# Optimization experiments

Measured on AMD Instinct MI355X. Metric: run time of the kernel, lower is better.

Reference implementation:

```python
import jax, jax.numpy as jnp
import numpy as np

B, L, DIN, D = 16, 1024, 512, 1024  # batch, l_max, input_dim, d_model
ORDER = 2


def setup_inputs() -> dict:
    key = jax.random.key(0)
    ks = jax.random.split(key, 8)
    n = lambda i, shape, sc: jax.random.normal(ks[i], shape, dtype=jnp.float32) * sc
    return {
        "x": n(0, (B, L, DIN), 1.0),
        # project_in (Linear since input_dim != output_dim)
        "Wp": n(1, (DIN, D), DIN ** -0.5),
        "bp": jnp.zeros((D,), jnp.float32),
        # hyena in_proj -> (order+1)*d channels
        "W_in": n(2, (D, 3 * D), D ** -0.5),
        "b_in": jnp.zeros((3 * D,), jnp.float32),
        # depthwise causal short conv, kernel 3
        "short_w": n(3, (3 * D, 1, 3), 0.5),
        "short_b": jnp.zeros((3 * D,), jnp.float32),
        # implicit long filters (materialized) + per-channel skip bias
        "k_filt": n(4, (ORDER, L, D), 0.02),
        "D_bias": n(5, (ORDER, D), 1.0),
        # hyena out_proj
        "W_out": n(6, (D, D), D ** -0.5),
        "b_out": jnp.zeros((D,), jnp.float32),
    }


def _fftconv(v, k, d_bias):
    # v: [B, L, d], k: [L, d] -> causal long conv via zero-padded FFT + skip
    n = 2 * v.shape[1]
    vf = jnp.fft.rfft(v.astype(jnp.float32), n=n, axis=1)
    kf = jnp.fft.rfft(k.astype(jnp.float32), n=n, axis=0)
    y = jnp.fft.irfft(vf * kf[None], n=n, axis=1)[:, : v.shape[1]]
    return (y + v * d_bias).astype(v.dtype)


def reference(x, Wp, bp, W_in, b_in, short_w, short_b, k_filt, D_bias, W_out, b_out):
    u = x @ Wp + bp                      # [B, L, D] project_in
    u = u @ W_in + b_in                  # [B, L, 3D]
    # depthwise causal short conv over sequence
    uc = jnp.transpose(u, (0, 2, 1))     # [B, 3D, L]
    uc = jax.lax.conv_general_dilated(
        uc, short_w, window_strides=(1,), padding=[(2, 0)],
        feature_group_count=3 * D, dimension_numbers=("NCH", "OIH", "NCH"),
    )[..., :L] + short_b[None, :, None]
    uc = jnp.transpose(uc, (0, 2, 1))    # [B, L, 3D]
    x1, x2, v = jnp.split(uc, 3, axis=-1)
    # Hyena recurrence: gate then long FFT conv, order=2
    v = _fftconv(v * x2, k_filt[0], D_bias[0])
    v = _fftconv(v * x1, k_filt[1], D_bias[1])
    return v @ W_out + b_out             # [B, L, D]
```

## Files before the change

### kernel.cpp

```cpp
#include <hip/hip_runtime.h>

#define BATCH 16
#define LSEQ 1024
#define DIN 512
#define DMODEL 1024
#define D3 3072
#define KCP 1064

typedef __attribute__((ext_vector_type(4))) float f32x4;
typedef __attribute__((ext_vector_type(8))) short bf16x8;

static __device__ __forceinline__ ushort f2bf(float f) {
    uint u = __float_as_uint(f);
    return (ushort)((u + 0x7FFFu + ((u >> 16) & 1u)) >> 16);
}
static __device__ __forceinline__ float bf2f(ushort h) {
    return __uint_as_float(((uint)h) << 16);
}

#define GLD16(ldst, gsrc)                                                        \
    __builtin_amdgcn_global_load_lds(                                            \
        (const __attribute__((address_space(1))) void*)(gsrc),                   \
        (__attribute__((address_space(3))) void*)(ldst), 16, 0, 0)

template <typename OutT, bool HAS_BIAS>
__global__ __launch_bounds__(512) void gemm_mfma(const ushort* __restrict__ A,
                                                 const ushort* __restrict__ Bt,
                                                 const float* __restrict__ bias,
                                                 OutT* __restrict__ C,
                                                 int M, int N, int K) {
    __shared__ ushort Als[3][256 * 32];
    __shared__ ushort Bls[3][128 * 32];
    int nwg = gridDim.x * gridDim.y;
    int bid = blockIdx.y * gridDim.x + blockIdx.x;
    bid = (bid & 7) * (nwg >> 3) + (bid >> 3);
    int n0 = (bid % gridDim.x) * 128, m0 = (bid / gridDim.x) * 256;
    int t = threadIdx.x;
    int w = t >> 6, l = t & 63;
    int wm = w >> 1, wn = w & 1;
    f32x4 acc[4][4] = {};

    int arow0 = 32 * w + (l >> 2);
    int kpart = (l & 3) * 8;
    const ushort* gA0 = A + (size_t)(m0 + arow0) * K + kpart;
    const ushort* gA1 = gA0 + (size_t)16 * K;
    const ushort* gB0 = Bt + (size_t)(n0 + 16 * w + (l >> 2)) * K + kpart;
    int soA = 1024 * w;
    int soB = 512 * w;

    int aoff = (wm * 64 + (l & 15)) * 32 + (l >> 4) * 8;
    int boff = (wn * 64 + (l & 15)) * 32 + (l >> 4) * 8;

#pragma unroll
    for (int s = 0; s < 2; s++) {
        GLD16(&Als[s][soA], gA0 + 32 * s);
        GLD16(&Als[s][soA + 512], gA1 + 32 * s);
        GLD16(&Bls[s][soB], gB0 + 32 * s);
    }

    int cur = 0;
    for (int k0 = 0; k0 < K; k0 += 32) {
        if (k0 + 32 < K)
            asm volatile("s_waitcnt vmcnt(3)" ::: "memory");
        else
            asm volatile("s_waitcnt vmcnt(0)" ::: "memory");
        __builtin_amdgcn_s_barrier();
        __builtin_amdgcn_sched_barrier(0);
        if (k0 + 64 < K) {
            int rf = cur >= 1 ? cur - 1 : 2;
            GLD16(&Als[rf][soA], gA0 + k0 + 64);
            GLD16(&Als[rf][soA + 512], gA1 + k0 + 64);
            GLD16(&Bls[rf][soB], gB0 + k0 + 64);
        }
        bf16x8 af[4], bg[4];
#pragma unroll
        for (int i = 0; i < 4; i++) af[i] = *(const bf16x8*)&Als[cur][aoff + i * 512];
#pragma unroll
        for (int j = 0; j < 4; j++) bg[j] = *(const bf16x8*)&Bls[cur][boff + j * 512];
#pragma unroll
        for (int i = 0; i < 4; i++)
#pragma unroll
            for (int j = 0; j < 4; j++)
                acc[i][j] = __builtin_amdgcn_mfma_f32_16x16x32_bf16(af[i], bg[j],
                                                                    acc[i][j], 0, 0, 0);
        cur = (cur == 2) ? 0 : cur + 1;
    }

#pragma unroll
    for (int j = 0; j < 4; j++) {
        int col = n0 + wn * 64 + 16 * j + (l & 15);
        float bv = HAS_BIAS ? bias[col] : 0.f;
#pragma unroll
        for (int i = 0; i < 4; i++) {
            int row0 = m0 + wm * 64 + 16 * i + (l >> 4) * 4;
#pragma unroll
            for (int r = 0; r < 4; r++) {
                float v = acc[i][j][r] + bv;
                if constexpr (sizeof(OutT) == 2)
                    C[(size_t)(row0 + r) * N + col] = (OutT)f2bf(v);
                else
                    C[(size_t)(row0 + r) * N + col] = (OutT)v;
            }
        }
    }
}

__global__ __launch_bounds__(512, 2) void conv_mfma(const ushort* __restrict__ At,
                                                    const ushort* __restrict__ X1t,
                                                    const float* __restrict__ kt,
                                                    const float* __restrict__ Db,
                                                    ushort* __restrict__ V2t, int nb) {
    __shared__ ushort a_lds[16 * 1024];
    __shared__ ushort kc[8 * KCP];
    int d = blockIdx.x;
    int tid = threadIdx.x;
    int w = tid >> 6, l = tid & 63;
    int lr = l & 15, lq = l >> 4;

    {
        int b = tid >> 5, s = tid & 31;
        const ushort* g = At + ((size_t)b * DMODEL + d) * LSEQ + s * 32;
#pragma unroll
        for (int j = 0; j < 4; j++) {
            uint4 v = {0u, 0u, 0u, 0u};
            if (b < nb) v = *(const uint4*)(g + 8 * j);
            int byte = (b * 1024 + s * 32 + 8 * j) * 2;
            *(uint4*)((char*)a_lds + (byte ^ (b << 4))) = v;
        }
    }

    int p = (7 - lr) & 7;
    int v0 = 1023 - lr + 8 * lq - p;
    int a_base = lr * 2048 + lq * 16;
    int swz = lr << 4;
    const int tis[4] = {w, 31 - w, 8 + w, 23 - w};
    int ti0 = tis[0], ti1 = tis[1], ti2 = tis[2], ti3 = tis[3];

    ushort gpre[4][2][4];
#pragma unroll
    for (int ii = 0; ii < 4; ii++)
#pragma unroll
        for (int h = 0; h < 2; h++)
#pragma unroll
            for (int r = 0; r < 4; r++) {
                int b = lq * 4 + r;
                int t2 = 32 * tis[ii] + 16 * h + lr;
                gpre[ii][h][r] = (b < nb)
                    ? X1t[((size_t)b * DMODEL + d) * LSEQ + t2] : (ushort)0;
            }

    for (int o = 0; o < 2; o++) {
        const float* krow = kt + ((size_t)o * DMODEL + d) * LSEQ;
        for (int idx = tid; idx < 8 * KCP; idx += 512) {
            int pp = idx / KCP;
            int u = idx - pp * KCP;
            int ki = 1023 - u - pp;
            kc[idx] = f2bf((ki >= 0) ? krow[ki] : 0.f);
        }
        __syncthreads();

        f32x4 a00 = {}, a01 = {}, a10 = {}, a11 = {};
        f32x4 a20 = {}, a21 = {}, a30 = {}, a31 = {};
        const char* kbp = (const char*)kc + ((size_t)p * KCP + v0) * 2;
        for (int m = 0; m < 32; m++) {
            bf16x8 b0 = *(const bf16x8*)(kbp - 64 * m);
            bf16x8 b1 = *(const bf16x8*)(kbp - 64 * m - 32);
            __builtin_amdgcn_s_setprio(1);
#define CSTEP(TI, A0, A1)                                                      \
            if ((TI) >= m) {                                                   \
                bf16x8 af = *(const bf16x8*)((const char*)a_lds +              \
                                             ((a_base + 64 * ((TI) - m)) ^ swz)); \
                A0 = __builtin_amdgcn_mfma_f32_16x16x32_bf16(af, b0, A0, 0, 0, 0); \
                A1 = __builtin_amdgcn_mfma_f32_16x16x32_bf16(af, b1, A1, 0, 0, 0); \
            }
            CSTEP(ti0, a00, a01)
            CSTEP(ti1, a10, a11)
            CSTEP(ti2, a20, a21)
            CSTEP(ti3, a30, a31)
#undef CSTEP
            __builtin_amdgcn_s_setprio(0);
        }
        float db = Db[o * DMODEL + d];
        __syncthreads();
#define CEPI(II, TI, AC, H)                                                    \
        {                                                                      \
            _Pragma("unroll")                                                  \
            for (int r = 0; r < 4; r++) {                                      \
                int t2 = 32 * (TI) + 16 * (H) + lr;                            \
                int b = lq * 4 + r;                                            \
                int ab = ((b * 1024 + t2) * 2) ^ (b << 4);                     \
                float a0v = bf2f(*(const ushort*)((const char*)a_lds + ab));   \
                float y = (AC)[r] + a0v * db;                                  \
                if (o == 0) y *= bf2f(gpre[II][H][r]);                         \
                *(ushort*)((char*)a_lds + ab) = f2bf(y);                       \
            }                                                                  \
        }
        CEPI(0, ti0, a00, 0) CEPI(0, ti0, a01, 1)
        CEPI(1, ti1, a10, 0) CEPI(1, ti1, a11, 1)
        CEPI(2, ti2, a20, 0) CEPI(2, ti2, a21, 1)
        CEPI(3, ti3, a30, 0) CEPI(3, ti3, a31, 1)
#undef CEPI
    }
    __syncthreads();
    {
        int b = tid >> 5, s = tid & 31;
        if (b < nb) {
            ushort* g = V2t + ((size_t)b * DMODEL + d) * LSEQ + s * 32;
#pragma unroll
            for (int j = 0; j < 4; j++) {
                int byte = (b * 1024 + s * 32 + 8 * j) * 2;
                uint4 v = *(const uint4*)((const char*)a_lds + (byte ^ (b << 4)));
                *(uint4*)(g + 8 * j) = v;
            }
        }
    }
}

__global__ void cvt_bf16(const float* __restrict__ in, ushort* __restrict__ out, int n4) {
    int i = blockIdx.x * blockDim.x + threadIdx.x;
    if (i >= n4) return;
    float4 v = *(const float4*)&in[4 * i];
    uint2 pk;
    pk.x = (uint)f2bf(v.x) | ((uint)f2bf(v.y) << 16);
    pk.y = (uint)f2bf(v.z) | ((uint)f2bf(v.w) << 16);
    *(uint2*)&out[4 * i] = pk;
}

__global__ void transpose_cvt(const float* __restrict__ in, ushort* __restrict__ out,
                              int R, int C) {
    __shared__ float tile[32][33];
    int c0 = blockIdx.x * 32, r0 = blockIdx.y * 32;
    int tx = threadIdx.x, ty = threadIdx.y;
#pragma unroll
    for (int i = 0; i < 4; i++)
        tile[ty + 8 * i][tx] = in[(size_t)(r0 + ty + 8 * i) * C + c0 + tx];
    __syncthreads();
#pragma unroll
    for (int i = 0; i < 4; i++)
        out[(size_t)(c0 + ty + 8 * i) * R + r0 + tx] = f2bf(tile[tx][ty + 8 * i]);
}

__global__ __launch_bounds__(256) void transpose_b16(const ushort* __restrict__ in,
                                                     ushort* __restrict__ out) {
    __shared__ uint tile[64][33];
    int t0 = blockIdx.x * 64, d0 = blockIdx.y * 64, b = blockIdx.z;
    int i = threadIdx.x;
    const ushort* ip = in + (size_t)b * DMODEL * LSEQ;
    ushort* op = out + (size_t)b * LSEQ * DMODEL;
    int dl = i >> 5, cu = i & 31;
#pragma unroll
    for (int j = 0; j < 8; j++)
        tile[dl + 8 * j][cu] =
            *(const uint*)&ip[(size_t)(d0 + dl + 8 * j) * LSEQ + t0 + 2 * cu];
    __syncthreads();
    int du = i & 31, tb = i >> 5;
#pragma unroll
    for (int j = 0; j < 8; j++) {
        int tl = tb + 8 * j;
        uint lo = (tile[2 * du][tl >> 1] >> (16 * (tl & 1))) & 0xFFFFu;
        uint hi = (tile[2 * du + 1][tl >> 1] >> (16 * (tl & 1))) & 0xFFFFu;
        *(uint*)&op[(size_t)(t0 + tl) * DMODEL + d0 + 2 * du] = lo | (hi << 16);
    }
}

__global__ void bias_fuse_part(const float* __restrict__ bp,
                               const float* __restrict__ W_in,
                               float* __restrict__ partial) {
    int n = blockIdx.x * 256 + threadIdx.x;
    int k0 = blockIdx.y * 128;
    float s = 0.f;
    for (int k = k0; k < k0 + 128; k++) s += bp[k] * W_in[(size_t)k * D3 + n];
    partial[(size_t)blockIdx.y * D3 + n] = s;
}
__global__ void bias_fuse_red(const float* __restrict__ partial,
                              const float* __restrict__ b_in,
                              float* __restrict__ bf) {
    int n = blockIdx.x * 256 + threadIdx.x;
    float s = b_in[n];
#pragma unroll
    for (int j = 0; j < 8; j++) s += partial[(size_t)j * D3 + n];
    bf[n] = s;
}

__global__ void transpose_k(const float* __restrict__ kf, float* __restrict__ kt) {
    __shared__ float tile[32][33];
    int s0 = blockIdx.x * 32, d0 = blockIdx.y * 32, o = blockIdx.z;
    int tx = threadIdx.x, ty = threadIdx.y;
#pragma unroll
    for (int i = 0; i < 4; i++)
        tile[ty + 8 * i][tx] = kf[((size_t)o * LSEQ + s0 + ty + 8 * i) * DMODEL + d0 + tx];
    __syncthreads();
#pragma unroll
    for (int i = 0; i < 4; i++)
        kt[((size_t)o * DMODEL + d0 + ty + 8 * i) * LSEQ + s0 + tx] = tile[tx][ty + 8 * i];
}

__global__ __launch_bounds__(256) void shortconv_gate(const ushort* __restrict__ UC,
                                                      const float* __restrict__ sw,
                                                      const float* __restrict__ sb,
                                                      ushort* __restrict__ At,
                                                      ushort* __restrict__ X1t) {
    __shared__ uint tin[3][34][33];
    __shared__ ushort oA[64][34];
    __shared__ ushort oX[64][34];
    int t0 = blockIdx.x * 32, c0 = blockIdx.y * 64, b = blockIdx.z;
    int tx = threadIdx.x, ty = threadIdx.y;
#pragma unroll
    for (int g = 0; g < 3; g++) {
        int ch = g * DMODEL + c0 + 2 * tx;
        for (int r = ty; r < 34; r += 8) {
            int t = t0 + r - 2;
            tin[g][r][tx] = (t >= 0)
                ? *(const uint*)&UC[((size_t)b * LSEQ + t) * D3 + ch] : 0u;
        }
    }
    __syncthreads();
    float2 res[3][4];
#pragma unroll
    for (int g = 0; g < 3; g++) {
        int ch = g * DMODEL + c0 + 2 * tx;
        float w00 = sw[ch * 3 + 0], w01 = sw[ch * 3 + 1], w02 = sw[ch * 3 + 2];
        float w10 = sw[ch * 3 + 3], w11 = sw[ch * 3 + 4], w12 = sw[ch * 3 + 5];
        float bb0 = sb[ch], bb1 = sb[ch + 1];
#pragma unroll
        for (int i = 0; i < 4; i++) {
            int r = ty + 8 * i + 2;
            uint u0 = tin[g][r - 2][tx], u1 = tin[g][r - 1][tx], u2 = tin[g][r][tx];
            res[g][i].x = w00 * bf2f((ushort)u0) + w01 * bf2f((ushort)u1) +
                          w02 * bf2f((ushort)u2) + bb0;
            res[g][i].y = w10 * bf2f((ushort)(u0 >> 16)) + w11 * bf2f((ushort)(u1 >> 16)) +
                          w12 * bf2f((ushort)(u2 >> 16)) + bb1;
        }
    }
#pragma unroll
    for (int i = 0; i < 4; i++) {
        int t = ty + 8 * i;
        oA[2 * tx][t]     = f2bf(res[2][i].x * res[1][i].x);
        oA[2 * tx + 1][t] = f2bf(res[2][i].y * res[1][i].y);
        oX[2 * tx][t]     = f2bf(res[0][i].x);
        oX[2 * tx + 1][t] = f2bf(res[0][i].y);
    }
    __syncthreads();
    int li = ty * 32 + tx;
    int row = li >> 2, cu0 = (li & 3) * 4;
    ushort* gA = At  + ((size_t)b * DMODEL + c0 + row) * LSEQ + t0;
    ushort* gX = X1t + ((size_t)b * DMODEL + c0 + row) * LSEQ + t0;
#pragma unroll
    for (int j = 0; j < 4; j++) {
        int cu = cu0 + j;
        uint av = (uint)oA[row][2 * cu] | ((uint)oA[row][2 * cu + 1] << 16);
        uint xv = (uint)oX[row][2 * cu] | ((uint)oX[row][2 * cu + 1] << 16);
        *(uint*)&gA[2 * cu] = av;
        *(uint*)&gX[2 * cu] = xv;
    }
}

extern "C" void kernel_launch(void* const* d_in, const int* in_sizes, int n_in,
                              void* d_out, int out_size, void* d_ws, size_t ws_size,
                              hipStream_t stream) {
    (void)in_sizes; (void)n_in; (void)out_size;
    const float* x    = (const float*)d_in[0];
    const float* Wp   = (const float*)d_in[1];
    const float* bp   = (const float*)d_in[2];
    const float* W_in = (const float*)d_in[3];
    const float* b_in = (const float*)d_in[4];
    const float* sw   = (const float*)d_in[5];
    const float* sb   = (const float*)d_in[6];
    const float* kf   = (const float*)d_in[7];
    const float* Db   = (const float*)d_in[8];
    const float* Wout = (const float*)d_in[9];
    const float* bout = (const float*)d_in[10];
    float* out = (float*)d_out;

    char* ws = (char*)d_ws;
    ushort* Wf_t   = (ushort*)(ws);
    float*  bfv    = (float*)(ws + 3145728);
    float*  kt     = (float*)(ws + 3162112);
    ushort* Wout_t = (ushort*)(ws + 11550720);
    const size_t PB = 13647872;

    const size_t XB  = 1048576;
    const size_t ATB = 2097152;
    const size_t X1B = 2097152;
    const size_t UCB = 6291456;
    const size_t V2B = 2097152;
    const size_t PREPB = 7471104;

    int cb = 1, cf = 1;
    {
        bool ok = false;
        for (int tcb = 16; tcb >= 1 && !ok; tcb >>= 1) {
            for (int tcf = tcb; tcf >= 1; tcf >>= 1) {
                size_t ucreg = (size_t)tcf * UCB;
                size_t v2need = (size_t)2 * tcb * V2B;
                if (ucreg < v2need) ucreg = v2need;
                if (ucreg < PREPB) ucreg = PREPB;
                size_t need = PB + (size_t)tcb * (XB + ATB + X1B) + ucreg;
                if (need <= ws_size) { cb = tcb; cf = tcf; ok = true; break; }
            }
        }
    }

    ushort* x_bf = (ushort*)(ws + PB);
    ushort* Atb  = (ushort*)(ws + PB + (size_t)cb * XB);
    ushort* X1tb = (ushort*)(ws + PB + (size_t)cb * (XB + ATB));
    char*   ucrg = ws + PB + (size_t)cb * (XB + ATB + X1B);
    ushort* UC   = (ushort*)ucrg;
    ushort* V2t  = (ushort*)ucrg;
    ushort* V2   = (ushort*)(ucrg + (size_t)cb * V2B);
    ushort* W_inT = (ushort*)ucrg;
    ushort* Wp_bf = (ushort*)(ucrg + 6291456);
    float*  bfp   = (float*)(ucrg + 7340032);

    transpose_cvt<<<dim3(96, 32), dim3(32, 8), 0, stream>>>(W_in, W_inT, DMODEL, D3);
    cvt_bf16<<<512, 256, 0, stream>>>(Wp, Wp_bf, DIN * DMODEL / 4);
    gemm_mfma<ushort, false><<<dim3(4, 12), 512, 0, stream>>>(W_inT, Wp_bf, nullptr,
                                                              Wf_t, D3, DIN, DMODEL);
    bias_fuse_part<<<dim3(12, 8), 256, 0, stream>>>(bp, W_in, bfp);
    bias_fuse_red<<<12, 256, 0, stream>>>(bfp, b_in, bfv);
    transpose_cvt<<<dim3(32, 32), dim3(32, 8), 0, stream>>>(Wout, Wout_t, DMODEL, DMODEL);
    transpose_k<<<dim3(32, 32, 2), dim3(32, 8), 0, stream>>>(kf, kt);

    for (int b0 = 0; b0 < BATCH; b0 += cb) {
        cvt_bf16<<<cb * LSEQ * DIN / 1024, 256, 0, stream>>>(
            x + (size_t)b0 * LSEQ * DIN, x_bf, cb * LSEQ * DIN / 4);
        for (int f0 = 0; f0 < cb; f0 += cf) {
            gemm_mfma<ushort, true><<<dim3(24, cf * 4), 512, 0, stream>>>(
                x_bf + (size_t)f0 * LSEQ * DIN, Wf_t, bfv, UC, cf * LSEQ, D3, DIN);
            shortconv_gate<<<dim3(32, 16, cf), dim3(32, 8), 0, stream>>>(
                UC, sw, sb, Atb + (size_t)f0 * DMODEL * LSEQ,
                X1tb + (size_t)f0 * DMODEL * LSEQ);
        }
        conv_mfma<<<DMODEL, 512, 0, stream>>>(Atb, X1tb, kt, Db, V2t, cb);
        transpose_b16<<<dim3(16, 16, cb), dim3(256), 0, stream>>>(V2t, V2);
        gemm_mfma<float, true><<<dim3(8, cb * 4), 512, 0, stream>>>(
            V2, Wout_t, bout, out + (size_t)b0 * LSEQ * DMODEL, cb * LSEQ, DMODEL, DMODEL);
    }
}
```

Baseline: 342.4 us.

## Rework GEMM main loop with 64-wide K tiles, XOR-swizzled LDS and split-phase staging

The bf16 MFMA GEMM now moves 64 elements of K per iteration instead of 32, staged through a triple-buffered LDS whose 16-byte chunks are XOR-swizzled to avoid bank conflicts on fragment reads. Each iteration runs two MFMA phases separated by barriers and issues the second half of the A prefetch between them, raising MFMA priority with s_setprio during compute. Launch bounds request two workgroups per CU. LDS use per block grows to 144 KB, which may not actually allow two blocks per CU, and the extra barrier per iteration adds synchronisation cost.

Measured after the change: 390.0 us. 13.9% more time.

```diff
diff --git a/kernel.cpp b/kernel.cpp
--- a/kernel.cpp
+++ b/kernel.cpp
@@ -24,13 +24,13 @@
         (__attribute__((address_space(3))) void*)(ldst), 16, 0, 0)
 
 template <typename OutT, bool HAS_BIAS>
-__global__ __launch_bounds__(512) void gemm_mfma(const ushort* __restrict__ A,
-                                                 const ushort* __restrict__ Bt,
-                                                 const float* __restrict__ bias,
-                                                 OutT* __restrict__ C,
-                                                 int M, int N, int K) {
-    __shared__ ushort Als[3][256 * 32];
-    __shared__ ushort Bls[3][128 * 32];
+__global__ __launch_bounds__(512, 2) void gemm_mfma(const ushort* __restrict__ A,
+                                                    const ushort* __restrict__ Bt,
+                                                    const float* __restrict__ bias,
+                                                    OutT* __restrict__ C,
+                                                    int M, int N, int K) {
+    __shared__ __align__(16) ushort Als[3 * 256 * 64];
+    __shared__ __align__(16) ushort Bls[3 * 128 * 64];
     int nwg = gridDim.x * gridDim.y;
     int bid = blockIdx.y * gridDim.x + blockIdx.x;
     bid = (bid & 7) * (nwg >> 3) + (bid >> 3);
@@ -38,61 +38,85 @@
     int t = threadIdx.x;
     int w = t >> 6, l = t & 63;
     int wm = w >> 1, wn = w & 1;
+    int lr = l & 15, lq = l >> 4;
     f32x4 acc[4][4] = {};
-
-    int arow0 = 32 * w + (l >> 2);
-    int kpart = (l & 3) * 8;
-    const ushort* gA0 = A + (size_t)(m0 + arow0) * K + kpart;
-    const ushort* gA1 = gA0 + (size_t)16 * K;
-    const ushort* gB0 = Bt + (size_t)(n0 + 16 * w + (l >> 2)) * K + kpart;
-    int soA = 1024 * w;
-    int soB = 512 * w;
-
-    int aoff = (wm * 64 + (l & 15)) * 32 + (l >> 4) * 8;
-    int boff = (wn * 64 + (l & 15)) * 32 + (l >> 4) * 8;
-
-#pragma unroll
-    for (int s = 0; s < 2; s++) {
-        GLD16(&Als[s][soA], gA0 + 32 * s);
-        GLD16(&Als[s][soA + 512], gA1 + 32 * s);
-        GLD16(&Bls[s][soB], gB0 + 32 * s);
-    }
-
-    int cur = 0;
-    for (int k0 = 0; k0 < K; k0 += 32) {
-        if (k0 + 32 < K)
-            asm volatile("s_waitcnt vmcnt(3)" ::: "memory");
+    int nK = K >> 6;
+
+    const ushort* Aptr = A + (size_t)m0 * K;
+    const ushort* Bptr = Bt + (size_t)n0 * K;
+
+#define STAGE_A(BUF, H, KT)                                                     \
+    {                                                                           \
+        _Pragma("unroll")                                                       \
+        for (int j = 0; j < 2; j++) {                                           \
+            int c = t + 512 * j;                                                \
+            GLD16(&Als[(BUF) * 16384 + (H) * 8192 + c * 8],                     \
+                  Aptr + (size_t)((H) * 128 + (c >> 3)) * K + (KT) * 64 +       \
+                      ((c & 7) ^ ((c >> 3) & 7)) * 8);                          \
+        }                                                                       \
+    }
+#define STAGE_B(BUF, KT)                                                        \
+    {                                                                           \
+        _Pragma("unroll")                                                       \
+        for (int j = 0; j < 2; j++) {                                           \
+            int c = t + 512 * j;                                                \
+            GLD16(&Bls[(BUF) * 8192 + c * 8],                                   \
+                  Bptr + (size_t)(c >> 3) * K + (KT) * 64 +                     \
+                      ((c & 7) ^ ((c >> 3) & 7)) * 8);                          \
+        }                                                                       \
+    }
+#define PHASE_MFMA(CUR, KH)                                                     \
+    {                                                                           \
+        bf16x8 af[4], bg[4];                                                    \
+        _Pragma("unroll")                                                       \
+        for (int i = 0; i < 4; i++)                                             \
+            af[i] = *(const bf16x8*)&Als[(CUR) * 16384 +                        \
+                (wm * 64 + 16 * i + lr) * 64 + ((lq + (KH) * 4) ^ (lr & 7)) * 8]; \
+        _Pragma("unroll")                                                       \
+        for (int j = 0; j < 4; j++)                                             \
+            bg[j] = *(const bf16x8*)&Bls[(CUR) * 8192 +                         \
+                (wn * 64 + 16 * j + lr) * 64 + ((lq + (KH) * 4) ^ (lr & 7)) * 8]; \
+        __builtin_amdgcn_s_setprio(1);                                          \
+        _Pragma("unroll")                                                       \
+        for (int i = 0; i < 4; i++)                                             \
+            _Pragma("unroll")                                                   \
+            for (int j = 0; j < 4; j++)                                         \
+                acc[i][j] = __builtin_amdgcn_mfma_f32_16x16x32_bf16(            \
+                    af[i], bg[j], acc[i][j], 0, 0, 0);                          \
+        __builtin_amdgcn_s_setprio(0);                                          \
+    }
+
+    STAGE_A(0, 0, 0) STAGE_B(0, 0) STAGE_A(0, 1, 0)
+    STAGE_A(1, 0, 1) STAGE_B(1, 1) STAGE_A(1, 1, 1)
+
+    for (int T = 0; T < nK; T++) {
+        int cur = T % 3;
+        int stg = (T + 2) % 3;
+        bool st = (T + 2) < nK;
+        if (st) { STAGE_A(stg, 0, T + 2) STAGE_B(stg, T + 2) }
+        if (T < nK - 1)
+            asm volatile("s_waitcnt vmcnt(6)" ::: "memory");
         else
             asm volatile("s_waitcnt vmcnt(0)" ::: "memory");
         __builtin_amdgcn_s_barrier();
         __builtin_amdgcn_sched_barrier(0);
-        if (k0 + 64 < K) {
-            int rf = cur >= 1 ? cur - 1 : 2;
-            GLD16(&Als[rf][soA], gA0 + k0 + 64);
-            GLD16(&Als[rf][soA + 512], gA1 + k0 + 64);
-            GLD16(&Bls[rf][soB], gB0 + k0 + 64);
-        }
-        bf16x8 af[4], bg[4];
-#pragma unroll
-        for (int i = 0; i < 4; i++) af[i] = *(const bf16x8*)&Als[cur][aoff + i * 512];
-#pragma unroll
-        for (int j = 0; j < 4; j++) bg[j] = *(const bf16x8*)&Bls[cur][boff + j * 512];
-#pragma unroll
-        for (int i = 0; i < 4; i++)
-#pragma unroll
-            for (int j = 0; j < 4; j++)
-                acc[i][j] = __builtin_amdgcn_mfma_f32_16x16x32_bf16(af[i], bg[j],
-                                                                    acc[i][j], 0, 0, 0);
-        cur = (cur == 2) ? 0 : cur + 1;
-    }
+        PHASE_MFMA(cur, 0)
+        __builtin_amdgcn_s_barrier();
+        if (st) { STAGE_A(stg, 1, T + 2) }
+        PHASE_MFMA(cur, 1)
+        __builtin_amdgcn_s_barrier();
+    }
+#undef STAGE_A
+#undef STAGE_B
+#undef PHASE_MFMA
 
 #pragma unroll
     for (int j = 0; j < 4; j++) {
-        int col = n0 + wn * 64 + 16 * j + (l & 15);
+        int col = n0 + wn * 64 + 16 * j + lr;
         float bv = HAS_BIAS ? bias[col] : 0.f;
 #pragma unroll
         for (int i = 0; i < 4; i++) {
-            int row0 = m0 + wm * 64 + 16 * i + (l >> 4) * 4;
+            int row0 = m0 + wm * 64 + 16 * i + lq * 4;
 #pragma unroll
             for (int r = 0; r < 4; r++) {
                 float v = acc[i][j][r] + bv;
```
